# Kernel tuning notes

Measured on AMD Instinct MI355X. Metric: run time of the kernel, lower is better.

The kernel has to match this reference:

```python
import jax, jax.numpy as jnp
import numpy as np
from jax import lax

K = 7          # neighborhood kernel size
NUM_HEADS = 4
EPS = 1e-5


def layernorm(x, w, b):
    mu = x.mean(-1, keepdims=True)
    var = ((x - mu) ** 2).mean(-1, keepdims=True)
    return (x - mu) * lax.rsqrt(var + EPS) * w + b


def window_idx(n, k):
    # NATTEN border behavior: window is shifted (not shrunk) at edges.
    start = jnp.clip(jnp.arange(n) - k // 2, 0, n - k)
    return start[:, None] + jnp.arange(k)  # [n, k]


def neighborhood_attention(x, qkv_w, qkv_b, rpb, proj_w, proj_b):
    B, H, W, C = x.shape
    nh, k = NUM_HEADS, K
    hd = C // nh
    scale = hd ** -0.5
    qkv = (x @ qkv_w + qkv_b).reshape(B, H, W, 3, nh, hd)
    q = jnp.transpose(qkv[:, :, :, 0], (0, 3, 1, 2, 4)) * scale  # [B,nh,H,W,hd]
    kk = jnp.transpose(qkv[:, :, :, 1], (0, 3, 1, 2, 4))
    vv = jnp.transpose(qkv[:, :, :, 2], (0, 3, 1, 2, 4))

    ri = window_idx(H, k)  # [H,k]
    ci = window_idx(W, k)  # [W,k]

    def gather(t):  # [B,nh,H,W,hd] -> [B,nh,H,W,k,k,hd]
        t = t[:, :, ri]           # [B,nh,H,k,W,hd]
        t = t[:, :, :, :, ci]     # [B,nh,H,k,W,k,hd]
        return jnp.transpose(t, (0, 1, 2, 4, 3, 5, 6))

    k_nb = gather(kk)
    v_nb = gather(vv).reshape(B, nh, H, W, k * k, hd)

    attn = jnp.einsum('bnhwd,bnhwijd->bnhwij', q, k_nb)  # [B,nh,H,W,k,k]

    # relative positional bias, rpb: [nh, 2k-1, 2k-1]
    br = ri - jnp.arange(H)[:, None] + (k - 1)  # [H,k] in [0, 2k-2]
    bc = ci - jnp.arange(W)[:, None] + (k - 1)  # [W,k]
    bias = rpb[:, br]                 # [nh,H,k,2k-1]
    bias = bias[:, :, :, bc]          # [nh,H,k,W,k]
    bias = jnp.transpose(bias, (0, 1, 3, 2, 4))  # [nh,H,W,k,k]

    attn = jax.nn.softmax((attn + bias[None]).reshape(B, nh, H, W, k * k), axis=-1)
    out = jnp.einsum('bnhwl,bnhwld->bnhwd', attn, v_nb)
    out = jnp.transpose(out, (0, 2, 3, 1, 4)).reshape(B, H, W, C)
    return out @ proj_w + proj_b


def mlp(x, w1, b1, w2, b2):
    return jax.nn.gelu(x @ w1 + b1, approximate=False) @ w2 + b2


def nat_block_forward(x, norm1_w, norm1_b, qkv_w, qkv_b, rpb, proj_w, proj_b,
                      norm2_w, norm2_b, fc1_w, fc1_b, fc2_w, fc2_b,
                      conv_w, dnorm_w, dnorm_b):
    depth = norm1_w.shape[0]
    for i in range(depth):
        h = layernorm(x, norm1_w[i], norm1_b[i])
        h = neighborhood_attention(h, qkv_w[i], qkv_b[i], rpb[i], proj_w[i], proj_b[i])
        x = x + h
        x = x + mlp(layernorm(x, norm2_w[i], norm2_b[i]),
                    fc1_w[i], fc1_b[i], fc2_w[i], fc2_b[i])
    # ConvDownsampler: 3x3 stride-2 conv (no bias) + LayerNorm, channels-last
    y = lax.conv_general_dilated(x, conv_w, (2, 2), ((1, 1), (1, 1)),
                                 dimension_numbers=('NHWC', 'HWIO', 'NHWC'))
    y = layernorm(y, dnorm_w, dnorm_b)
    return (y, x)


def setup_inputs() -> dict:
    key = jax.random.key(0)
    ks = jax.random.split(key, 12)
    B, H, W, C = 2, 56, 56, 128
    depth, nh, k = 2, NUM_HEADS, K
    hidden = 4 * C
    init = lambda kk, shape: jax.random.normal(kk, shape, jnp.float32) * 0.02
    return {
        'x': jax.random.normal(ks[0], (B, H, W, C), jnp.float32),
        'norm1_w': jnp.ones((depth, C), jnp.float32),
        'norm1_b': jnp.zeros((depth, C), jnp.float32),
        'qkv_w': init(ks[1], (depth, C, 3 * C)),
        'qkv_b': jnp.zeros((depth, 3 * C), jnp.float32),
        'rpb': init(ks[2], (depth, nh, 2 * k - 1, 2 * k - 1)),
        'proj_w': init(ks[3], (depth, C, C)),
        'proj_b': jnp.zeros((depth, C), jnp.float32),
        'norm2_w': jnp.ones((depth, C), jnp.float32),
        'norm2_b': jnp.zeros((depth, C), jnp.float32),
        'fc1_w': init(ks[4], (depth, C, hidden)),
        'fc1_b': jnp.zeros((depth, hidden), jnp.float32),
        'fc2_w': init(ks[5], (depth, hidden, C)),
        'fc2_b': jnp.zeros((depth, C), jnp.float32),
        'conv_w': init(ks[6], (3, 3, C, 2 * C)),
        'dnorm_w': jnp.ones((2 * C,), jnp.float32),
        'dnorm_b': jnp.zeros((2 * C,), jnp.float32),
    }


def reference(x, norm1_w, norm1_b, qkv_w, qkv_b, rpb, proj_w, proj_b,
              norm2_w, norm2_b, fc1_w, fc1_b, fc2_w, fc2_b,
              conv_w, dnorm_w, dnorm_b):
    return nat_block_forward(x, norm1_w, norm1_b, qkv_w, qkv_b, rpb, proj_w,
                             proj_b, norm2_w, norm2_b, fc1_w, fc1_b, fc2_w,
                             fc2_b, conv_w, dnorm_w, dnorm_b)
```

## Files before the change

kernel.cpp:

```cpp
#include <hip/hip_runtime.h>
#include <stdint.h>


typedef __attribute__((ext_vector_type(8))) short bf16x8;
typedef __attribute__((ext_vector_type(4))) float f32x4;

__device__ __forceinline__ float bf2f(uint16_t u) {
  union { uint32_t u; float f; } t;
  t.u = (uint32_t)u << 16;
  return t.f;
}
__device__ __forceinline__ uint16_t f2bf(float f) {
  union { float f; uint32_t u; } t;
  t.f = f;
  return (uint16_t)((t.u + 0x7FFFu + ((t.u >> 16) & 1u)) >> 16);
}

struct PrepArgs {
  const float* src[9];
  uint16_t* dst[9];
  int K[9], N[9];
  int cum[10];
};

__global__ __launch_bounds__(256) void prep_weights(PrepArgs a) {
  __shared__ float t[32][33];
  int bt = blockIdx.x;
  int j = 0;
#pragma unroll
  for (int u = 0; u < 9; ++u)
    if (bt >= a.cum[u + 1]) j = u + 1;
  int lt = bt - a.cum[j];
  const float* w = a.src[j];
  uint16_t* wt = a.dst[j];
  int K = a.K[j], N = a.N[j];
  int tn = N >> 5;
  int n0 = (lt % tn) * 32, k0 = (lt / tn) * 32;
  int tx = threadIdx.x & 31, ty = threadIdx.x >> 5;
#pragma unroll
  for (int r2 = 0; r2 < 32; r2 += 8)
    t[ty + r2][tx] = w[(size_t)(k0 + ty + r2) * N + n0 + tx];
  __syncthreads();
#pragma unroll
  for (int r2 = 0; r2 < 32; r2 += 8)
    wt[(size_t)(n0 + ty + r2) * K + k0 + tx] = f2bf(t[tx][ty + r2]);
}

__global__ __launch_bounds__(256) void ln256_kernel(const float* __restrict__ p0,
                                                    const float* __restrict__ p1,
                                                    const float* __restrict__ p2,
                                                    float* __restrict__ out,
                                                    const float* __restrict__ w,
                                                    const float* __restrict__ b) {
  int wave = threadIdx.x >> 6, lane = threadIdx.x & 63;
  int pix = blockIdx.x * 4 + wave;
  size_t base = (size_t)pix * 256 + lane * 4;
  float4 a0 = *(const float4*)(p0 + base);
  float4 a1 = *(const float4*)(p1 + base);
  float4 a2 = *(const float4*)(p2 + base);
  float4 v;
  v.x = a0.x + a1.x + a2.x;
  v.y = a0.y + a1.y + a2.y;
  v.z = a0.z + a1.z + a2.z;
  v.w = a0.w + a1.w + a2.w;
  float s = v.x + v.y + v.z + v.w;
  float s2 = v.x * v.x + v.y * v.y + v.z * v.z + v.w * v.w;
#pragma unroll
  for (int off = 32; off; off >>= 1) {
    s += __shfl_xor(s, off, 64);
    s2 += __shfl_xor(s2, off, 64);
  }
  float mu = s * (1.f / 256.f);
  float var = s2 * (1.f / 256.f) - mu * mu;
  float r = rsqrtf(var + 1e-5f);
  float4 wv = *(const float4*)(w + lane * 4);
  float4 bv = *(const float4*)(b + lane * 4);
  float4 o;
  o.x = (v.x - mu) * r * wv.x + bv.x;
  o.y = (v.y - mu) * r * wv.y + bv.y;
  o.z = (v.z - mu) * r * wv.z + bv.z;
  o.w = (v.w - mu) * r * wv.w + bv.w;
  *(float4*)(out + base) = o;
}

template <int KD, int ND, int ACT, int RES, int OUTB, int LNF>
__global__ __launch_bounds__(256) void mfma_gemm32(
    const uint16_t* __restrict__ A, const float* __restrict__ Af,
    const float* __restrict__ lnw, const float* __restrict__ lnb,
    const uint16_t* __restrict__ Wt, const float* __restrict__ bias,
    const float* __restrict__ res, float* __restrict__ outf,
    uint16_t* __restrict__ outb, float* __restrict__ outf2, int M) {
  __shared__ __align__(16) char smem[26112];
  uint16_t(*sA)[136] = (uint16_t(*)[136])smem;
  uint16_t(*sB)[136] = (uint16_t(*)[136])(smem + 8704);
  float(*sC)[68] = (float(*)[68])smem;

  int m0 = blockIdx.x * 32, n0 = blockIdx.y * 64;
  int tid = threadIdx.x, lane = tid & 63, wid = tid >> 6;
  int wr = (wid >> 1) * 16, wc = (wid & 1) * 32;
  int lc = lane & 15, g = lane >> 4;
  int lko = g * 8;

  f32x4 acc0 = {0.f, 0.f, 0.f, 0.f}, acc1 = acc0;

  constexpr int NCH = KD / 128;
#pragma unroll
  for (int c = 0; c < NCH; ++c) {
    if constexpr (LNF) {
      int r = tid >> 3, qt = tid & 7;
      const float4* xr = (const float4*)(Af + (size_t)(m0 + r) * 128 + qt * 16);
      float4 xv[4];
      float s = 0.f, s2 = 0.f;
#pragma unroll
      for (int u = 0; u < 4; ++u) {
        xv[u] = xr[u];
        s += xv[u].x + xv[u].y + xv[u].z + xv[u].w;
        s2 += xv[u].x * xv[u].x + xv[u].y * xv[u].y + xv[u].z * xv[u].z + xv[u].w * xv[u].w;
      }
      s += __shfl_xor(s, 1, 64);
      s += __shfl_xor(s, 2, 64);
      s += __shfl_xor(s, 4, 64);
      s2 += __shfl_xor(s2, 1, 64);
      s2 += __shfl_xor(s2, 2, 64);
      s2 += __shfl_xor(s2, 4, 64);
      float mu = s * (1.f / 128.f);
      float var = s2 * (1.f / 128.f) - mu * mu;
      float rstd = rsqrtf(var + 1e-5f);
      const float* lw = lnw + qt * 16;
      const float* lb = lnb + qt * 16;
      union { uint16_t us[8]; bf16x8 v; } tq[2];
#pragma unroll
      for (int u = 0; u < 4; ++u) {
        tq[u >> 1].us[(u & 1) * 4 + 0] = f2bf((xv[u].x - mu) * rstd * lw[u * 4 + 0] + lb[u * 4 + 0]);
        tq[u >> 1].us[(u & 1) * 4 + 1] = f2bf((xv[u].y - mu) * rstd * lw[u * 4 + 1] + lb[u * 4 + 1]);
        tq[u >> 1].us[(u & 1) * 4 + 2] = f2bf((xv[u].z - mu) * rstd * lw[u * 4 + 2] + lb[u * 4 + 2]);
        tq[u >> 1].us[(u & 1) * 4 + 3] = f2bf((xv[u].w - mu) * rstd * lw[u * 4 + 3] + lb[u * 4 + 3]);
      }
      *(bf16x8*)&sA[r][qt * 16] = tq[0].v;
      *(bf16x8*)&sA[r][qt * 16 + 8] = tq[1].v;
    } else {
#pragma unroll
      for (int it = 0; it < 2; ++it) {
        int chunk = tid + it * 256;
        int row = chunk >> 4, kc = (chunk & 15) * 8;
        *(bf16x8*)&sA[row][kc] =
            *(const bf16x8*)(A + (size_t)(m0 + row) * KD + c * 128 + kc);
      }
    }
#pragma unroll
    for (int it = 0; it < 4; ++it) {
      int chunk = tid + it * 256;
      int row = chunk >> 4, kc = (chunk & 15) * 8;
      *(bf16x8*)&sB[row][kc] =
          *(const bf16x8*)(Wt + (size_t)(n0 + row) * KD + c * 128 + kc);
    }
    __syncthreads();
#pragma unroll
    for (int kk = 0; kk < 128; kk += 32) {
      bf16x8 a0 = *(const bf16x8*)&sA[wr + lc][kk + lko];
      bf16x8 b0 = *(const bf16x8*)&sB[wc + lc][kk + lko];
      bf16x8 b1 = *(const bf16x8*)&sB[wc + 16 + lc][kk + lko];
      acc0 = __builtin_amdgcn_mfma_f32_16x16x32_bf16(a0, b0, acc0, 0, 0, 0);
      acc1 = __builtin_amdgcn_mfma_f32_16x16x32_bf16(a0, b1, acc1, 0, 0, 0);
    }
    __syncthreads();
  }

  {
    float bv0 = bias ? bias[n0 + wc + lc] : 0.f;
    float bv1 = bias ? bias[n0 + wc + lc + 16] : 0.f;
#pragma unroll
    for (int ni = 0; ni < 2; ++ni) {
      float bv = ni ? bv1 : bv0;
      f32x4 av = ni ? acc1 : acc0;
#pragma unroll
      for (int j = 0; j < 4; ++j) {
        float a = av[j] + bv;
        if (ACT) a = 0.5f * a * (1.f + erff(a * 0.70710678118654752f));
        sC[wr + g * 4 + j][wc + ni * 16 + lc] = a;
      }
    }
    __syncthreads();
    int r = tid >> 3, cs = (tid & 7) * 8;
    int grow = m0 + r;
    if (grow < M) {
      const float4* cp = (const float4*)&sC[r][cs];
      float4 c4[2] = {cp[0], cp[1]};
      if (RES) {
        const float4* rp = (const float4*)(res + (size_t)grow * ND + n0 + cs);
#pragma unroll
        for (int u = 0; u < 2; ++u) {
          float4 rv = rp[u];
          c4[u].x += rv.x; c4[u].y += rv.y; c4[u].z += rv.z; c4[u].w += rv.w;
        }
      }
      if (OUTB) {
        union { uint16_t us[8]; bf16x8 v; } t;
#pragma unroll
        for (int u = 0; u < 2; ++u) {
          t.us[u * 4 + 0] = f2bf(c4[u].x);
          t.us[u * 4 + 1] = f2bf(c4[u].y);
          t.us[u * 4 + 2] = f2bf(c4[u].z);
          t.us[u * 4 + 3] = f2bf(c4[u].w);
        }
        *(bf16x8*)(outb + (size_t)grow * ND + n0 + cs) = t.v;
      } else {
        float4* op = (float4*)(outf + (size_t)grow * ND + n0 + cs);
        op[0] = c4[0];
        op[1] = c4[1];
        if (outf2) {
          float4* op2 = (float4*)(outf2 + (size_t)grow * ND + n0 + cs);
          op2[0] = c4[0];
          op2[1] = c4[1];
        }
      }
    }
  }
}

__global__ __launch_bounds__(512) void mlp_fused2(
    const uint16_t* __restrict__ att,
    const float* __restrict__ xin,
    const uint16_t* __restrict__ pwt,
    const float* __restrict__ pb,
    const float* __restrict__ n2w, const float* __restrict__ n2b,
    const uint16_t* __restrict__ f1wt,
    const float* __restrict__ f1b,
    const uint16_t* __restrict__ f2wt,
    const float* __restrict__ f2b,
    float* __restrict__ xout,
    float* __restrict__ out2) {
  __shared__ __align__(16) uint16_t sW[128][136];
  __shared__ __align__(16) uint16_t sA[16][136];
  __shared__ __align__(16) float sY[16][132];
  __shared__ __align__(16) char sHraw[16640];
  uint16_t(*sH)[520] = (uint16_t(*)[520])sHraw;
  float(*sC)[132] = (float(*)[132])sHraw;

  const f32x4 fz = {0.f, 0.f, 0.f, 0.f};
  int m0 = blockIdx.x * 16;
  int tid = threadIdx.x;
  int lane = tid & 63, wid = tid >> 6;
  int lc = lane & 15, g = lane >> 4;
  int rr = tid >> 5, cc = tid & 31;

  float4 rx = *(const float4*)(xin + (size_t)(m0 + rr) * 128 + cc * 4);

  if (tid < 256) {
    int r = tid >> 4, q = tid & 15;
    *(bf16x8*)&sA[r][q * 8] = *(const bf16x8*)(att + (size_t)(m0 + r) * 128 + q * 8);
  }
#pragma unroll
  for (int it = 0; it < 4; ++it) {
    int chunk = tid + it * 512;
    int row = chunk >> 4, q = chunk & 15;
    *(bf16x8*)&sW[row][q * 8] = *(const bf16x8*)(pwt + (size_t)row * 128 + q * 8);
  }
  __syncthreads();

  {
    f32x4 acc = fz;
#pragma unroll
    for (int ks = 0; ks < 4; ++ks) {
      bf16x8 a = *(const bf16x8*)&sA[lc][ks * 32 + g * 8];
      bf16x8 b = *(const bf16x8*)&sW[wid * 16 + lc][ks * 32 + g * 8];
      acc = __builtin_amdgcn_mfma_f32_16x16x32_bf16(a, b, acc, 0, 0, 0);
    }
    float bv = pb[wid * 16 + lc];
#pragma unroll
    for (int j = 0; j < 4; ++j) sY[g * 4 + j][wid * 16 + lc] = acc[j] + bv;
  }
  __syncthreads();

  {
    float4 sv = *(const float4*)&sY[rr][cc * 4];
    float4 y;
    y.x = sv.x + rx.x; y.y = sv.y + rx.y; y.z = sv.z + rx.z; y.w = sv.w + rx.w;
    float s = y.x + y.y + y.z + y.w;
    float s2 = y.x * y.x + y.y * y.y + y.z * y.z + y.w * y.w;
#pragma unroll
    for (int off = 1; off < 32; off <<= 1) {
      s += __shfl_xor(s, off, 64);
      s2 += __shfl_xor(s2, off, 64);
    }
    float mu = s * (1.f / 128.f);
    float var = s2 * (1.f / 128.f) - mu * mu;
    float rstd = rsqrtf(var + 1e-5f);
    *(float4*)&sY[rr][cc * 4] = y;
    float4 lw = *(const float4*)(n2w + cc * 4);
    float4 lb = *(const float4*)(n2b + cc * 4);
    ushort4 nv;
    nv.x = f2bf((y.x - mu) * rstd * lw.x + lb.x);
    nv.y = f2bf((y.y - mu) * rstd * lw.y + lb.y);
    nv.z = f2bf((y.z - mu) * rstd * lw.z + lb.z);
    nv.w = f2bf((y.w - mu) * rstd * lw.w + lb.w);
    *(ushort4*)&sA[rr][cc * 4] = nv;
  }
  __syncthreads();

#pragma unroll 1
  for (int ch = 0; ch < 4; ++ch) {
#pragma unroll
    for (int it = 0; it < 4; ++it) {
      int chunk = tid + it * 512;
      int row = chunk >> 4, q = chunk & 15;
      *(bf16x8*)&sW[row][q * 8] =
          *(const bf16x8*)(f1wt + (size_t)(ch * 128 + row) * 128 + q * 8);
    }
    __syncthreads();
    f32x4 acc = fz;
#pragma unroll
    for (int ks = 0; ks < 4; ++ks) {
      bf16x8 a = *(const bf16x8*)&sA[lc][ks * 32 + g * 8];
      bf16x8 b = *(const bf16x8*)&sW[wid * 16 + lc][ks * 32 + g * 8];
      acc = __builtin_amdgcn_mfma_f32_16x16x32_bf16(a, b, acc, 0, 0, 0);
    }
    int col = ch * 128 + wid * 16 + lc;
    float bv = f1b[col];
#pragma unroll
    for (int j = 0; j < 4; ++j) {
      float h = acc[j] + bv;
      h = 0.5f * h * (1.f + erff(h * 0.70710678118654752f));
      sH[g * 4 + j][col] = f2bf(h);
    }
    __syncthreads();
  }

  f32x4 acc2 = fz;
#pragma unroll 1
  for (int ch = 0; ch < 4; ++ch) {
#pragma unroll
    for (int it = 0; it < 4; ++it) {
      int chunk = tid + it * 512;
      int row = chunk >> 4, q = chunk & 15;
      *(bf16x8*)&sW[row][q * 8] =
          *(const bf16x8*)(f2wt + (size_t)row * 512 + ch * 128 + q * 8);
    }
    __syncthreads();
#pragma unroll
    for (int ks = 0; ks < 4; ++ks) {
      bf16x8 a = *(const bf16x8*)&sH[lc][ch * 128 + ks * 32 + g * 8];
      bf16x8 b = *(const bf16x8*)&sW[wid * 16 + lc][ks * 32 + g * 8];
      acc2 = __builtin_amdgcn_mfma_f32_16x16x32_bf16(a, b, acc2, 0, 0, 0);
    }
    __syncthreads();
  }

  {
    int col = wid * 16 + lc;
    float bv = f2b[col];
#pragma unroll
    for (int j = 0; j < 4; ++j) sC[g * 4 + j][col] = acc2[j] + bv;
  }
  __syncthreads();

  {
    float4 cv = *(const float4*)&sC[rr][cc * 4];
    float4 yv = *(const float4*)&sY[rr][cc * 4];
    float4 o;
    o.x = cv.x + yv.x; o.y = cv.y + yv.y; o.z = cv.z + yv.z; o.w = cv.w + yv.w;
    *(float4*)(xout + (size_t)(m0 + rr) * 128 + cc * 4) = o;
    if (out2) *(float4*)(out2 + (size_t)(m0 + rr) * 128 + cc * 4) = o;
  }
}

#define KSWZ(row, colbytes) (((row) * 64 + (colbytes)) ^ (((row) & 7) << 4))

__global__ __launch_bounds__(128) void natten_mfma(const uint16_t* __restrict__ qkv,
                                                   const float* __restrict__ rpb,
                                                   uint16_t* __restrict__ out) {
  __shared__ uint16_t s_k[144 * 32];
  __shared__ uint16_t s_vt[32][168];
  __shared__ uint16_t s_p[32][168];
  __shared__ float s_rpb[169];

  int tid = threadIdx.x;
  int blk = blockIdx.x;
  int bh = blk & 7, tile = blk >> 3;
  int b = bh >> 2, head = bh & 3;
  int ti = tile / 7, tj = tile % 7;
  int i0 = ti * 4, j0 = tj * 8;
  int rbase = min(max(i0 - 3, 0), 46);
  int cbase = min(max(j0 - 3, 0), 42);

  const bf16x8 bz = {0, 0, 0, 0, 0, 0, 0, 0};
  const f32x4 fz = {0.f, 0.f, 0.f, 0.f};

  if (tid < 16)
    *(bf16x8*)((char*)s_k + KSWZ(140 + (tid >> 2), (tid & 3) * 16)) = bz;
  for (int idx = tid; idx < 640; idx += 128) s_vt[idx & 31][140 + (idx >> 5)] = 0;
  for (int idx = tid; idx < 512; idx += 128) s_p[idx & 31][144 + (idx >> 5)] = 0;
  for (int idx = tid; idx < 560; idx += 128) {
    int pos = idx >> 2, ch = (idx & 3) * 8;
    int r = rbase + pos / 14, c = cbase + pos % 14;
    const uint16_t* base = qkv + ((size_t)(b * 3136 + r * 56 + c)) * 384 + head * 32 + ch;
    bf16x8 kv = *(const bf16x8*)(base + 128);
    bf16x8 vv = *(const bf16x8*)(base + 256);
    *(bf16x8*)((char*)s_k + KSWZ(pos, ch * 2)) = kv;
#pragma unroll
    for (int e = 0; e < 8; ++e) s_vt[ch + e][pos] = (uint16_t)vv[e];
  }
  for (int idx = tid; idx < 169; idx += 128) s_rpb[idx] = rpb[head * 169 + idx];
  __syncthreads();

  int lane = tid & 63, wq = tid >> 6;
  int lc = lane & 15, g = lane >> 4;
  int q0 = wq * 16;

  int pA = q0 + lc;
  int piA = i0 + (pA >> 3), pjA = j0 + (pA & 7);
  bf16x8 qfrag =
      *(const bf16x8*)(qkv + ((size_t)(b * 3136 + piA * 56 + pjA)) * 384 + head * 32 + g * 8);

  f32x4 S[9];
#pragma unroll
  for (int t = 0; t < 9; ++t) {
    bf16x8 kfrag = *(const bf16x8*)((char*)s_k + KSWZ(t * 16 + lc, g * 16));
    S[t] = __builtin_amdgcn_mfma_f32_16x16x32_bf16(qfrag, kfrag, fz, 0, 0, 0);
  }

  int qi = wq * 2 + (g >> 1);
  int i = i0 + qi;
  int a = min(max(i - 3, 0), 49) - rbase;
  int brc = 6 - (i0 - rbase) - qi;
  int bj[4], bcc[4];
#pragma unroll
  for (int jj = 0; jj < 4; ++jj) {
    int qj = 4 * (g & 1) + jj;
    int j = j0 + qj;
    bj[jj] = min(max(j - 3, 0), 49) - cbase;
    bcc[jj] = 6 - (j0 - cbase) - qj;
  }

  float mx[4] = {-1e30f, -1e30f, -1e30f, -1e30f};
  int kr = (lc >= 14) ? 1 : 0;
  int kc = lc - 14 * kr;
#pragma unroll
  for (int t = 0; t < 9; ++t) {
    bool vr = (kr >= a) && (kr <= a + 6);
    int brrow = (kr + brc) * 13;
#pragma unroll
    for (int jj = 0; jj < 4; ++jj) {
      float sv = S[t][jj] * 0.17677669529663687f;
      bool v = vr && (kc >= bj[jj]) && (kc <= bj[jj] + 6);
      int bidx = v ? (brrow + kc + bcc[jj]) : 0;
      float val = v ? (sv + s_rpb[bidx]) : -1e30f;
      S[t][jj] = val;
      mx[jj] = fmaxf(mx[jj], val);
    }
    kr += 1;
    kc += 2;
    if (kc >= 14) { kc -= 14; kr += 1; }
  }
#pragma unroll
  for (int jj = 0; jj < 4; ++jj) {
#pragma unroll
    for (int off = 1; off < 16; off <<= 1) mx[jj] = fmaxf(mx[jj], __shfl_xor(mx[jj], off, 64));
  }

  float sm[4] = {0.f, 0.f, 0.f, 0.f};
#pragma unroll
  for (int t = 0; t < 9; ++t) {
#pragma unroll
    for (int jj = 0; jj < 4; ++jj) {
      float e = __expf(S[t][jj] - mx[jj]);
      sm[jj] += e;
      s_p[q0 + g * 4 + jj][t * 16 + lc] = f2bf(e);
    }
  }
#pragma unroll
  for (int jj = 0; jj < 4; ++jj) {
#pragma unroll
    for (int off = 1; off < 16; off <<= 1) sm[jj] += __shfl_xor(sm[jj], off, 64);
    sm[jj] = 1.f / sm[jj];
  }

  __syncthreads();

  f32x4 O[2] = {fz, fz};
#pragma unroll
  for (int ks = 0; ks < 5; ++ks) {
    bf16x8 pa = *(const bf16x8*)&s_p[q0 + lc][ks * 32 + g * 8];
#pragma unroll
    for (int dt = 0; dt < 2; ++dt) {
      bf16x8 vb = *(const bf16x8*)&s_vt[dt * 16 + lc][ks * 32 + g * 8];
      O[dt] = __builtin_amdgcn_mfma_f32_16x16x32_bf16(pa, vb, O[dt], 0, 0, 0);
    }
  }

#pragma unroll
  for (int jj = 0; jj < 4; ++jj) {
    int q = q0 + g * 4 + jj;
    int pi = i0 + (q >> 3), pj = j0 + (q & 7);
    size_t ob = ((size_t)(b * 3136 + pi * 56 + pj)) * 128 + head * 32;
    out[ob + lc] = f2bf(O[0][jj] * sm[jj]);
    out[ob + 16 + lc] = f2bf(O[1][jj] * sm[jj]);
  }
}

__global__ __launch_bounds__(256) void conv_gemm32(const float* __restrict__ x,
                                                   const uint16_t* __restrict__ Wt,
                                                   float* __restrict__ parts) {
  __shared__ __align__(16) char smem[26112];
  uint16_t(*sA)[136] = (uint16_t(*)[136])smem;
  uint16_t(*sB)[136] = (uint16_t(*)[136])(smem + 8704);
  float(*sC)[68] = (float(*)[68])smem;

  int m0 = blockIdx.x * 32, n0 = blockIdx.y * 64, kh = blockIdx.z;
  float* part = parts + (size_t)kh * 1568 * 256;
  int tid = threadIdx.x, lane = tid & 63, wid = tid >> 6;
  int wr = (wid >> 1) * 16, wc = (wid & 1) * 32;
  int lc = lane & 15, g = lane >> 4;
  int lko = g * 8;

  f32x4 acc0 = {0.f, 0.f, 0.f, 0.f}, acc1 = acc0;

  int r = tid >> 3, qt = tid & 7;
  int opix = m0 + r;
  int ow = opix % 28, oh = (opix / 28) % 28, bb = opix / 784;
  int ih = 2 * oh - 1 + kh;
  bool rowok = (ih >= 0) && (ih < 56);

#pragma unroll
  for (int kwc = 0; kwc < 3; ++kwc) {
    int iw = 2 * ow - 1 + kwc;
    float4 xv[4] = {{0.f, 0.f, 0.f, 0.f}, {0.f, 0.f, 0.f, 0.f},
                    {0.f, 0.f, 0.f, 0.f}, {0.f, 0.f, 0.f, 0.f}};
    if (rowok && iw >= 0 && iw < 56) {
      const float4* p =
          (const float4*)(x + (size_t)((bb * 56 + ih) * 56 + iw) * 128 + qt * 16);
#pragma unroll
      for (int u = 0; u < 4; ++u) xv[u] = p[u];
    }
    union { uint16_t us[8]; bf16x8 v; } tq[2];
#pragma unroll
    for (int u = 0; u < 4; ++u) {
      tq[u >> 1].us[(u & 1) * 4 + 0] = f2bf(xv[u].x);
      tq[u >> 1].us[(u & 1) * 4 + 1] = f2bf(xv[u].y);
      tq[u >> 1].us[(u & 1) * 4 + 2] = f2bf(xv[u].z);
      tq[u >> 1].us[(u & 1) * 4 + 3] = f2bf(xv[u].w);
    }
    *(bf16x8*)&sA[r][qt * 16] = tq[0].v;
    *(bf16x8*)&sA[r][qt * 16 + 8] = tq[1].v;
#pragma unroll
    for (int it = 0; it < 4; ++it) {
      int chunk = tid + it * 256;
      int row = chunk >> 4, kc = (chunk & 15) * 8;
      *(bf16x8*)&sB[row][kc] =
          *(const bf16x8*)(Wt + (size_t)(n0 + row) * 1152 + kh * 384 + kwc * 128 + kc);
    }
    __syncthreads();
#pragma unroll
    for (int kk = 0; kk < 128; kk += 32) {
      bf16x8 a0 = *(const bf16x8*)&sA[wr + lc][kk + lko];
      bf16x8 b0 = *(const bf16x8*)&sB[wc + lc][kk + lko];
      bf16x8 b1 = *(const bf16x8*)&sB[wc + 16 + lc][kk + lko];
      acc0 = __builtin_amdgcn_mfma_f32_16x16x32_bf16(a0, b0, acc0, 0, 0, 0);
      acc1 = __builtin_amdgcn_mfma_f32_16x16x32_bf16(a0, b1, acc1, 0, 0, 0);
    }
    __syncthreads();
  }

#pragma unroll
  for (int ni = 0; ni < 2; ++ni) {
    f32x4 av = ni ? acc1 : acc0;
#pragma unroll
    for (int j = 0; j < 4; ++j) sC[wr + g * 4 + j][wc + ni * 16 + lc] = av[j];
  }
  __syncthreads();
  int rr = tid >> 3, cs = (tid & 7) * 8;
  int grow = m0 + rr;
  if (grow < 1568) {
    const float4* cp = (const float4*)&sC[rr][cs];
    float4* op = (float4*)(part + (size_t)grow * 256 + n0 + cs);
    op[0] = cp[0];
    op[1] = cp[1];
  }
}

extern "C" void kernel_launch(void* const* d_in, const int* in_sizes, int n_in,
                              void* d_out, int out_size, void* d_ws, size_t ws_size,
                              hipStream_t stream) {
  const float* x    = (const float*)d_in[0];
  const float* n1w  = (const float*)d_in[1];
  const float* n1b  = (const float*)d_in[2];
  const float* qkvw = (const float*)d_in[3];
  const float* qkvb = (const float*)d_in[4];
  const float* rpb  = (const float*)d_in[5];
  const float* pw   = (const float*)d_in[6];
  const float* pb   = (const float*)d_in[7];
  const float* n2w  = (const float*)d_in[8];
  const float* n2b  = (const float*)d_in[9];
  const float* f1w  = (const float*)d_in[10];
  const float* f1b  = (const float*)d_in[11];
  const float* f2w  = (const float*)d_in[12];
  const float* f2b  = (const float*)d_in[13];
  const float* cw   = (const float*)d_in[14];
  const float* dnw  = (const float*)d_in[15];
  const float* dnb  = (const float*)d_in[16];
  float* out = (float*)d_out;

  char* wsb = (char*)d_ws;
  float*    xbuf    = (float*)(wsb + 0);
  uint16_t* qkv_b   = (uint16_t*)(wsb + 3211264);
  uint16_t* att_b   = (uint16_t*)(wsb + 8028160);
  float*    parts   = (float*)(wsb + 16056320);
  uint16_t* wts     = (uint16_t*)(wsb + 20873216);
  uint16_t* qkvwt = wts;
  uint16_t* pwt   = wts + 98304;
  uint16_t* f1wt  = wts + 131072;
  uint16_t* f2wt  = wts + 262144;
  uint16_t* cwt   = wts + 393216;

  PrepArgs pa;
  pa.src[0] = qkvw;         pa.dst[0] = qkvwt;          pa.K[0] = 128; pa.N[0] = 384;
  pa.src[1] = qkvw + 49152; pa.dst[1] = qkvwt + 49152;  pa.K[1] = 128; pa.N[1] = 384;
  pa.src[2] = pw;           pa.dst[2] = pwt;            pa.K[2] = 128; pa.N[2] = 128;
  pa.src[3] = pw + 16384;   pa.dst[3] = pwt + 16384;    pa.K[3] = 128; pa.N[3] = 128;
  pa.src[4] = f1w;          pa.dst[4] = f1wt;           pa.K[4] = 128; pa.N[4] = 512;
  pa.src[5] = f1w + 65536;  pa.dst[5] = f1wt + 65536;   pa.K[5] = 128; pa.N[5] = 512;
  pa.src[6] = f2w;          pa.dst[6] = f2wt;           pa.K[6] = 512; pa.N[6] = 128;
  pa.src[7] = f2w + 65536;  pa.dst[7] = f2wt + 65536;   pa.K[7] = 512; pa.N[7] = 128;
  pa.src[8] = cw;           pa.dst[8] = cwt;            pa.K[8] = 1152; pa.N[8] = 256;
  int cums[10] = {0, 48, 96, 112, 128, 192, 256, 320, 384, 672};
  for (int u = 0; u < 10; ++u) pa.cum[u] = cums[u];
  prep_weights<<<672, 256, 0, stream>>>(pa);

  for (int i = 0; i < 2; ++i) {
    const float* xin = (i == 0) ? x : xbuf;
    mfma_gemm32<128, 384, 0, 0, 1, 1><<<dim3(196, 6), 256, 0, stream>>>(
        nullptr, xin, n1w + i * 128, n1b + i * 128, qkvwt + i * 49152, qkvb + i * 384,
        nullptr, nullptr, qkv_b, nullptr, 6272);
    natten_mfma<<<784, 128, 0, stream>>>(qkv_b, rpb + i * 676, att_b);
    mlp_fused2<<<392, 512, 0, stream>>>(
        att_b, xin, pwt + i * 16384, pb + i * 128, n2w + i * 128, n2b + i * 128,
        f1wt + i * 65536, f1b + i * 512, f2wt + i * 65536, f2b + i * 128,
        xbuf, (i == 1) ? (out + 401408) : nullptr);
  }

  conv_gemm32<<<dim3(49, 4, 3), 256, 0, stream>>>(xbuf, cwt, parts);
  ln256_kernel<<<392, 256, 0, stream>>>(parts, parts + 401408, parts + 802816, out, dnw, dnb);
}
```

Measured before the change: 87.30 us.

## Fuse second-layer LayerNorm and QKV projection into first MLP kernel epilogue

The first block's MLP kernel now also applies the next block's norm1 LayerNorm to its output rows and computes the 384-wide QKV projection with MFMA, writing bf16 qkv directly. This removes one separate QKV GEMM launch and the re-read of the residual stream from global memory. In exchange, the 16-row tile kernel does extra serial work (three weight chunk loads with barriers), using only 392 blocks, which may be less efficient than the standalone GEMM's grid.

```diff
diff --git a/kernel.cpp b/kernel.cpp
--- a/kernel.cpp
+++ b/kernel.cpp
@@ -218,6 +218,7 @@
   }
 }
 
+template <int WQKV>
 __global__ __launch_bounds__(512) void mlp_fused2(
     const uint16_t* __restrict__ att,
     const float* __restrict__ xin,
@@ -229,7 +230,11 @@
     const uint16_t* __restrict__ f2wt,
     const float* __restrict__ f2b,
     float* __restrict__ xout,
-    float* __restrict__ out2) {
+    float* __restrict__ out2,
+    const float* __restrict__ n1w, const float* __restrict__ n1b,
+    const uint16_t* __restrict__ qwt,
+    const float* __restrict__ qb,
+    uint16_t* __restrict__ qkvout) {
   __shared__ __align__(16) uint16_t sW[128][136];
   __shared__ __align__(16) uint16_t sA[16][136];
   __shared__ __align__(16) float sY[16][132];
@@ -361,6 +366,57 @@
     o.x = cv.x + yv.x; o.y = cv.y + yv.y; o.z = cv.z + yv.z; o.w = cv.w + yv.w;
     *(float4*)(xout + (size_t)(m0 + rr) * 128 + cc * 4) = o;
     if (out2) *(float4*)(out2 + (size_t)(m0 + rr) * 128 + cc * 4) = o;
+    if constexpr (WQKV) {
+      float s = o.x + o.y + o.z + o.w;
+      float s2 = o.x * o.x + o.y * o.y + o.z * o.z + o.w * o.w;
+#pragma unroll
+      for (int off = 1; off < 32; off <<= 1) {
+        s += __shfl_xor(s, off, 64);
+        s2 += __shfl_xor(s2, off, 64);
+      }
+      float mu = s * (1.f / 128.f);
+      float var = s2 * (1.f / 128.f) - mu * mu;
+      float rstd = rsqrtf(var + 1e-5f);
+      float4 lw = *(const float4*)(n1w + cc * 4);
+      float4 lb = *(const float4*)(n1b + cc * 4);
+      ushort4 nv;
+      nv.x = f2bf((o.x - mu) * rstd * lw.x + lb.x);
+      nv.y = f2bf((o.y - mu) * rstd * lw.y + lb.y);
+      nv.z = f2bf((o.z - mu) * rstd * lw.z + lb.z);
+      nv.w = f2bf((o.w - mu) * rstd * lw.w + lb.w);
+      *(ushort4*)&sA[rr][cc * 4] = nv;
+    }
+  }
+
+  if constexpr (WQKV) {
+#pragma unroll 1
+    for (int ch = 0; ch < 3; ++ch) {
+#pragma unroll
+      for (int it = 0; it < 4; ++it) {
+        int chunk = tid + it * 512;
+        int row = chunk >> 4, q = chunk & 15;
+        *(bf16x8*)&sW[row][q * 8] =
+            *(const bf16x8*)(qwt + (size_t)(ch * 128 + row) * 128 + q * 8);
+      }
+      __syncthreads();
+      f32x4 acc = fz;
+#pragma unroll
+      for (int ks = 0; ks < 4; ++ks) {
+        bf16x8 a = *(const bf16x8*)&sA[lc][ks * 32 + g * 8];
+        bf16x8 b = *(const bf16x8*)&sW[wid * 16 + lc][ks * 32 + g * 8];
+        acc = __builtin_amdgcn_mfma_f32_16x16x32_bf16(a, b, acc, 0, 0, 0);
+      }
+      int col = ch * 128 + wid * 16 + lc;
+      float bv = qb[col];
+#pragma unroll
+      for (int j = 0; j < 4; ++j) sH[g * 4 + j][col] = f2bf(acc[j] + bv);
+      __syncthreads();
+    }
+    for (int idx = tid; idx < 1536; idx += 512) {
+      int row = idx / 96, colc = (idx % 96) * 4;
+      *(ushort4*)(qkvout + (size_t)(m0 + row) * 384 + colc) =
+          *(const ushort4*)&sH[row][colc];
+    }
   }
 }
 
@@ -626,17 +682,17 @@
   for (int u = 0; u < 10; ++u) pa.cum[u] = cums[u];
   prep_weights<<<672, 256, 0, stream>>>(pa);
 
-  for (int i = 0; i < 2; ++i) {
-    const float* xin = (i == 0) ? x : xbuf;
-    mfma_gemm32<128, 384, 0, 0, 1, 1><<<dim3(196, 6), 256, 0, stream>>>(
-        nullptr, xin, n1w + i * 128, n1b + i * 128, qkvwt + i * 49152, qkvb + i * 384,
-        nullptr, nullptr, qkv_b, nullptr, 6272);
-    natten_mfma<<<784, 128, 0, stream>>>(qkv_b, rpb + i * 676, att_b);
-    mlp_fused2<<<392, 512, 0, stream>>>(
-        att_b, xin, pwt + i * 16384, pb + i * 128, n2w + i * 128, n2b + i * 128,
-        f1wt + i * 65536, f1b + i * 512, f2wt + i * 65536, f2b + i * 128,
-        xbuf, (i == 1) ? (out + 401408) : nullptr);
-  }
+  mfma_gemm32<128, 384, 0, 0, 1, 1><<<dim3(196, 6), 256, 0, stream>>>(
+      nullptr, x, n1w, n1b, qkvwt, qkvb, nullptr, nullptr, qkv_b, nullptr, 6272);
+  natten_mfma<<<784, 128, 0, stream>>>(qkv_b, rpb, att_b);
+  mlp_fused2<1><<<392, 512, 0, stream>>>(
+      att_b, x, pwt, pb, n2w, n2b, f1wt, f1b, f2wt, f2b, xbuf, nullptr,
+      n1w + 128, n1b + 128, qkvwt + 49152, qkvb + 384, qkv_b);
+  natten_mfma<<<784, 128, 0, stream>>>(qkv_b, rpb + 676, att_b);
+  mlp_fused2<0><<<392, 512, 0, stream>>>(
+      att_b, xbuf, pwt + 16384, pb + 128, n2w + 128, n2b + 128,
+      f1wt + 65536, f1b + 512, f2wt + 65536, f2b + 128, xbuf, out + 401408,
+      nullptr, nullptr, nullptr, nullptr, nullptr);
 
   conv_gemm32<<<dim3(49, 4, 3), 256, 0, stream>>>(xbuf, cwt, parts);
   ln256_kernel<<<392, 256, 0, stream>>>(parts, parts + 401408, parts + 802816, out, dnw, dnb);
```

Measured after the change: 83.62 us, median of 3. 1.04x faster.
